# Kernel optimization log

Measured on AMD Instinct MI355X. Metric: run time of the kernel, lower is better.

## Reference

```python
import jax, jax.numpy as jnp
import numpy as np

T, B, D, H = 2048, 4, 1024, 16
DK = D // H
SCALE = 1.0 / np.sqrt(DK)


def setup_inputs() -> dict:
    key = jax.random.key(0)
    k1, k2, k3 = jax.random.split(key, 3)
    x = jax.random.normal(k1, (T, B, D), dtype=jnp.float32)
    # xavier_uniform-ish scaling
    W_qkv = jax.random.normal(k2, (3 * D, D), dtype=jnp.float32) * np.sqrt(2.0 / (D + 3 * D))
    W_out = jax.random.normal(k3, (D, D), dtype=jnp.float32) * np.sqrt(1.0 / D)
    b_out = jnp.zeros((D,), dtype=jnp.float32)
    return {"x": x, "W_qkv": W_qkv, "W_out": W_out, "b_out": b_out}


def reference(x, W_qkv, W_out, b_out):
    Tn, Bn, Dn = x.shape
    # QKV projection (Linear with weight [3D, D], no bias)
    qkv = x @ W_qkv.T                                  # (T, B, 3D)
    qkv = qkv.reshape(Tn, Bn, 3, H, DK)
    q, k, v = qkv[:, :, 0], qkv[:, :, 1], qkv[:, :, 2]  # each (T, B, H, dk)
    scores = jnp.einsum('tbhd,sbhd->bhts', q, k) * SCALE  # (B, H, T, T)
    causal = jnp.triu(jnp.ones((Tn, Tn), dtype=bool), k=1)
    scores = jnp.where(causal, -jnp.inf, scores)
    attn = jax.nn.softmax(scores, axis=-1)
    out = jnp.einsum('bhts,sbhd->tbhd', attn, v)        # (T, B, H, dk)
    out = out.reshape(Tn, Bn, Dn)
    return out @ W_out.T + b_out
```

## Files before the change

### kernel.cpp

```cpp
#include <hip/hip_runtime.h>
#include <stdint.h>

#define T_DIM 2048
#define B_DIM 4
#define D_DIM 1024
#define H_NUM 16
#define HD 64
#define MROWS (T_DIM * B_DIM)
#define QKV_N (3 * D_DIM)
#define ATT_C 0.18033688011112042f

typedef unsigned short u16;
typedef __bf16 bf16x8 __attribute__((ext_vector_type(8)));
typedef float f32x4 __attribute__((ext_vector_type(4)));
typedef float f32x16 __attribute__((ext_vector_type(16)));
typedef u16 u16x4 __attribute__((ext_vector_type(4)));
typedef u16 u16x8 __attribute__((ext_vector_type(8)));

__device__ __forceinline__ u16 f2bf(float f) {
  union { float f; unsigned u; } v; v.f = f;
  unsigned r = v.u + 0x7fffu + ((v.u >> 16) & 1u);
  return (u16)(r >> 16);
}

__device__ __forceinline__ void async_copy16(void* lds, const void* g) {
  __builtin_amdgcn_global_load_lds((__attribute__((address_space(1))) void*)(g),
                                   (__attribute__((address_space(3))) void*)(lds),
                                   16, 0, 0);
}

__global__ __launch_bounds__(256) void cast3_f32_bf16(
    const float* __restrict__ s0, const float* __restrict__ s1,
    const float* __restrict__ s2, u16* __restrict__ dst,
    int n0, int n01, int ntot4) {
  int i = blockIdx.x * 256 + threadIdx.x;
  if (i >= ntot4) return;
  int e = i * 4;
  const float* s; int off;
  if (e < n0) { s = s0; off = 0; }
  else if (e < n01) { s = s1; off = n0; }
  else { s = s2; off = n01; }
  float4 v = *reinterpret_cast<const float4*>(s + (e - off));
  u16x4 o = {f2bf(v.x), f2bf(v.y), f2bf(v.z), f2bf(v.w)};
  *reinterpret_cast<u16x4*>(dst + e) = o;
}

template <int OUT_F32_BIAS>
__global__ __launch_bounds__(256) void gemm_bt(
    const u16* __restrict__ A, const u16* __restrict__ Bm,
    u16* __restrict__ Cb, float* __restrict__ Cf, const float* __restrict__ bias,
    int M, int N, int K) {
  __shared__ __attribute__((aligned(16))) u16 As[128 * 64];
  __shared__ __attribute__((aligned(16))) u16 Bs[128 * 64];

  const int tid = threadIdx.x;
  const int lane = tid & 63, wid = tid >> 6;
  const int l15 = lane & 15, lg = lane >> 4;
  const int wr = wid >> 1, wc = wid & 1;
  const int m0 = blockIdx.y * 128, n0 = blockIdx.x * 128;

  f32x4 acc[4][4];
#pragma unroll
  for (int i = 0; i < 4; i++)
#pragma unroll
    for (int j = 0; j < 4; j++) acc[i][j] = (f32x4){0.f, 0.f, 0.f, 0.f};

  const int srow = tid >> 3;
  const int scol = (tid & 7) * 8;
  const u16* gA = A + (size_t)(m0 + srow) * K + scol;
  const u16* gB = Bm + (size_t)(n0 + srow) * K + scol;
  u16* lA = As + tid * 8;
  u16* lB = Bs + tid * 8;

  const int KT = K >> 6;
  for (int kt = 0; kt < KT; ++kt) {
    const int kofs = kt * 64;
#pragma unroll
    for (int p = 0; p < 4; ++p) {
      async_copy16(lA + p * 256 * 8, gA + (size_t)(p * 32) * K + kofs);
      async_copy16(lB + p * 256 * 8, gB + (size_t)(p * 32) * K + kofs);
    }
    __syncthreads();
#pragma unroll
    for (int kk = 0; kk < 2; ++kk) {
      bf16x8 af[4], bfr[4];
#pragma unroll
      for (int mt = 0; mt < 4; ++mt)
        af[mt] = *reinterpret_cast<const bf16x8*>(
            &As[(wr * 64 + mt * 16 + l15) * 64 + kk * 32 + lg * 8]);
#pragma unroll
      for (int nt = 0; nt < 4; ++nt)
        bfr[nt] = *reinterpret_cast<const bf16x8*>(
            &Bs[(wc * 64 + nt * 16 + l15) * 64 + kk * 32 + lg * 8]);
#pragma unroll
      for (int mt = 0; mt < 4; ++mt)
#pragma unroll
        for (int nt = 0; nt < 4; ++nt)
          acc[mt][nt] = __builtin_amdgcn_mfma_f32_16x16x32_bf16(
              af[mt], bfr[nt], acc[mt][nt], 0, 0, 0);
    }
    __syncthreads();
  }

  const float qsc = (!OUT_F32_BIAS && n0 < D_DIM) ? ATT_C : 1.0f;
#pragma unroll
  for (int mt = 0; mt < 4; ++mt) {
#pragma unroll
    for (int r = 0; r < 4; ++r) {
      const int row = m0 + wr * 64 + mt * 16 + lg * 4 + r;
#pragma unroll
      for (int nt = 0; nt < 4; ++nt) {
        const int col = n0 + wc * 64 + nt * 16 + l15;
        float v = acc[mt][nt][r];
        if (OUT_F32_BIAS) {
          Cf[(size_t)row * N + col] = v + bias[col];
        } else {
          Cb[(size_t)row * N + col] = f2bf(v * qsc);
        }
      }
    }
  }
}

#define VF_STRIDE 24
#define VF_FRAG (32 * VF_STRIDE)

__device__ __forceinline__ void process32(
    const bf16x8 (&qf)[4], f32x16 (&o)[2], f32x16& lacc,
    int q0w, int kv0, int l31, int hi, bool needMask, const bf16x8 onesf,
    const u16* __restrict__ Ks, const u16* __restrict__ Vf) {
  f32x16 s[2];
#pragma unroll
  for (int kb = 0; kb < 2; ++kb)
#pragma unroll
    for (int r = 0; r < 16; ++r) s[kb][r] = 0.f;

  __builtin_amdgcn_s_setprio(1);
#pragma unroll
  for (int kb = 0; kb < 2; ++kb) {
#pragma unroll
    for (int ks = 0; ks < 4; ++ks) {
      const int row = kb * 32 + l31;
      bf16x8 kf = *reinterpret_cast<const bf16x8*>(
          &Ks[row * 64 + ((((ks << 1) | hi)) ^ (l31 & 7)) * 8]);
      s[kb] = __builtin_amdgcn_mfma_f32_32x32x16_bf16(kf, qf[ks], s[kb], 0, 0, 0);
    }
  }
  __builtin_amdgcn_s_setprio(0);

  if (needMask) {
    const int q = q0w + l31;
#pragma unroll
    for (int kb = 0; kb < 2; ++kb)
#pragma unroll
      for (int r = 0; r < 16; ++r) {
        const int kv = kv0 + kb * 32 + (r & 3) + ((r >> 2) << 3) + (hi << 2);
        if (kv > q) s[kb][r] = -1e30f;
      }
  }
#pragma unroll
  for (int kb = 0; kb < 2; ++kb)
#pragma unroll
    for (int r = 0; r < 16; ++r)
      s[kb][r] = __builtin_amdgcn_exp2f(s[kb][r]);

  union Frag { unsigned u[4]; bf16x8 v; };
  Frag pf[4];
#pragma unroll
  for (int kb = 0; kb < 2; ++kb)
#pragma unroll
    for (int g = 0; g < 2; ++g) {
#pragma unroll
      for (int t2 = 0; t2 < 2; ++t2) {
        unsigned x, y;
        asm("v_cvt_pk_bf16_f32 %0, %1, %2"
            : "=v"(x) : "v"(s[kb][g * 8 + t2 * 2]), "v"(s[kb][g * 8 + t2 * 2 + 1]));
        asm("v_cvt_pk_bf16_f32 %0, %1, %2"
            : "=v"(y) : "v"(s[kb][g * 8 + t2 * 2 + 4]), "v"(s[kb][g * 8 + t2 * 2 + 5]));
        asm("v_permlane32_swap_b32 %0, %1" : "+v"(x), "+v"(y));
        pf[kb * 2 + g].u[t2] = x;
        pf[kb * 2 + g].u[t2 + 2] = y;
      }
    }

  __builtin_amdgcn_s_setprio(1);
#pragma unroll
  for (int ks = 0; ks < 4; ++ks) {
    lacc = __builtin_amdgcn_mfma_f32_32x32x16_bf16(onesf, pf[ks].v, lacc, 0, 0, 0);
#pragma unroll
    for (int db = 0; db < 2; ++db) {
      bf16x8 vf = *reinterpret_cast<const bf16x8*>(
          &Vf[(ks * 2 + db) * VF_FRAG + l31 * VF_STRIDE + hi * 8]);
      o[db] = __builtin_amdgcn_mfma_f32_32x32x16_bf16(vf, pf[ks].v, o[db], 0, 0, 0);
    }
  }
  __builtin_amdgcn_s_setprio(0);
}

__global__ __launch_bounds__(256, 2) void attn_kernel(
    const u16* __restrict__ qkv, u16* __restrict__ aout) {
  __shared__ __attribute__((aligned(16))) u16 Ks[128 * 64];
  __shared__ __attribute__((aligned(16))) u16 Vf[16 * VF_FRAG];

  const int tid = threadIdx.x;
  const int lane = tid & 63, w = tid >> 6;
  const int l31 = lane & 31, hi = lane >> 5;

  const int nwg = gridDim.x * gridDim.y;
  const int lin = blockIdx.y * gridDim.x + blockIdx.x;
  const int swz = (lin & 7) * (nwg >> 3) + (lin >> 3);
  const int px = swz % gridDim.x;
  const int bh = swz / gridDim.x;
  const int b = bh >> 4, h = bh & 15;
  const int qtA = px, qtB = 15 - px;
  const int q0A = qtA * 128 + w * 32, q0B = qtB * 128 + w * 32;

  bf16x8 qfA[4], qfB[4];
  {
    const u16* pA = qkv + ((size_t)(q0A + l31) * B_DIM + b) * QKV_N + h * HD + hi * 8;
    const u16* pB = qkv + ((size_t)(q0B + l31) * B_DIM + b) * QKV_N + h * HD + hi * 8;
#pragma unroll
    for (int ks = 0; ks < 4; ++ks) {
      qfA[ks] = *reinterpret_cast<const bf16x8*>(pA + ks * 16);
      qfB[ks] = *reinterpret_cast<const bf16x8*>(pB + ks * 16);
    }
  }

  bf16x8 onesf;
  {
    union { u16 u[8]; bf16x8 v; } ou;
#pragma unroll
    for (int i = 0; i < 8; ++i) ou.u[i] = 0x3F80;
    onesf = ou.v;
  }

  f32x16 oA[2], oB[2], laccA, laccB;
#pragma unroll
  for (int r = 0; r < 16; ++r) { laccA[r] = 0.f; laccB[r] = 0.f; }
#pragma unroll
  for (int db = 0; db < 2; ++db)
#pragma unroll
    for (int r = 0; r < 16; ++r) { oA[db][r] = 0.f; oB[db][r] = 0.f; }

  const int srow = tid >> 3;
  const int scol = (tid & 7) * 8;
  const int csw = (tid & 7) ^ (srow & 7);

  for (int kt2 = 0; kt2 <= qtB; ++kt2) {
    const int base = kt2 * 128;
#pragma unroll
    for (int p = 0; p < 4; ++p) {
      const u16* gK = qkv + ((size_t)(base + p * 32 + srow) * B_DIM + b) * QKV_N +
                      D_DIM + h * HD + csw * 8;
      async_copy16(Ks + tid * 8 + p * 2048, gK);
    }
    u16x8 vv[4];
#pragma unroll
    for (int p = 0; p < 4; ++p) {
      const u16* gV = qkv + ((size_t)(base + p * 32 + srow) * B_DIM + b) * QKV_N +
                      2 * D_DIM + h * HD + scol;
      vv[p] = *reinterpret_cast<const u16x8*>(gV);
    }
#pragma unroll
    for (int p = 0; p < 4; ++p) {
      const int kvl = p * 32 + srow;
      const int fb = (kvl >> 4) * 2;
      const int e16 = kvl & 15;
#pragma unroll
      for (int jj = 0; jj < 8; ++jj) {
        const int j = (jj + srow) & 7;
        const int d = scol + j;
        Vf[(fb + (d >> 5)) * VF_FRAG + (d & 31) * VF_STRIDE + e16] = vv[p][j];
      }
    }
    __syncthreads();

#pragma unroll
    for (int half = 0; half < 2; ++half) {
      const int kv0 = base + half * 64;
      const u16* Kh = Ks + half * (64 * 64);
      const u16* Vh = Vf + half * 8 * VF_FRAG;
      if (kv0 <= q0A + 31)
        process32(qfA, oA, laccA, q0A, kv0, l31, hi, kv0 + 63 > q0A, onesf, Kh, Vh);
      if (kv0 <= q0B + 31)
        process32(qfB, oB, laccB, q0B, kv0, l31, hi, kv0 + 63 > q0B, onesf, Kh, Vh);
    }
    __syncthreads();
  }

#pragma unroll
  for (int t = 0; t < 2; ++t) {
    const float inv = 1.0f / (t == 0 ? laccA[0] : laccB[0]);
    const int q0w = t == 0 ? q0A : q0B;
    f32x16* o = t == 0 ? oA : oB;
    u16* orow = aout + ((size_t)(q0w + l31) * B_DIM + b) * D_DIM + h * HD;
#pragma unroll
    for (int db = 0; db < 2; ++db)
#pragma unroll
      for (int rq = 0; rq < 4; ++rq) {
        u16x4 o4;
#pragma unroll
        for (int e = 0; e < 4; ++e) o4[e] = f2bf(o[db][rq * 4 + e] * inv);
        *reinterpret_cast<u16x4*>(orow + db * 32 + rq * 8 + hi * 4) = o4;
      }
  }
}

extern "C" void kernel_launch(void* const* d_in, const int* in_sizes, int n_in,
                              void* d_out, int out_size, void* d_ws, size_t ws_size,
                              hipStream_t stream) {
  (void)in_sizes; (void)n_in; (void)out_size; (void)ws_size;
  const float* x = (const float*)d_in[0];
  const float* Wqkv = (const float*)d_in[1];
  const float* Wout = (const float*)d_in[2];
  const float* bout = (const float*)d_in[3];
  float* out = (float*)d_out;

  u16* xb = (u16*)d_ws;
  u16* wqkvb = xb + (size_t)MROWS * D_DIM;
  u16* woutb = wqkvb + (size_t)QKV_N * D_DIM;
  u16* qkv = woutb + (size_t)D_DIM * D_DIM;
  u16* aout = qkv + (size_t)MROWS * QKV_N;

  {
    const int n0 = MROWS * D_DIM;
    const int n01 = n0 + QKV_N * D_DIM;
    const int ntot = n01 + D_DIM * D_DIM;
    const int n4 = ntot / 4;
    cast3_f32_bf16<<<(n4 + 255) / 256, 256, 0, stream>>>(
        x, Wqkv, Wout, xb, n0, n01, n4);
  }

  gemm_bt<0><<<dim3(QKV_N / 128, MROWS / 128), 256, 0, stream>>>(
      xb, wqkvb, qkv, nullptr, nullptr, MROWS, QKV_N, D_DIM);

  attn_kernel<<<dim3(8, B_DIM * H_NUM), 256, 0, stream>>>(qkv, aout);

  gemm_bt<1><<<dim3(D_DIM / 128, MROWS / 128), 256, 0, stream>>>(
      aout, woutb, nullptr, out, bout, MROWS, D_DIM, D_DIM);
}
```

Baseline: 192.9 us.

## Replace QKV GEMM with 256x256 tiled, 8-wave pipelined async-copy kernel

Adds a dedicated QKV projection kernel that uses 256x256 output tiles, 512 threads, 128KB dynamic LDS double-buffered with async global-to-LDS copies, XOR-swizzled LDS layout and an interleaved schedule of LDS loads, prefetches and MFMA quarters separated by barriers. A grid swizzle groups workgroups for better L2 reuse. The Q scaling moves from the generic GEMM into this kernel. The aim is higher MFMA utilization and less load latency exposure in the largest GEMM, at the cost of one workgroup per CU and more barriers.

```diff
diff --git a/kernel.cpp b/kernel.cpp
--- a/kernel.cpp
+++ b/kernel.cpp
@@ -102,7 +102,6 @@
     __syncthreads();
   }
 
-  const float qsc = (!OUT_F32_BIAS && n0 < D_DIM) ? ATT_C : 1.0f;
 #pragma unroll
   for (int mt = 0; mt < 4; ++mt) {
 #pragma unroll
@@ -115,11 +114,171 @@
         if (OUT_F32_BIAS) {
           Cf[(size_t)row * N + col] = v + bias[col];
         } else {
-          Cb[(size_t)row * N + col] = f2bf(v * qsc);
+          Cb[(size_t)row * N + col] = f2bf(v);
         }
       }
     }
   }
+}
+
+__global__ __launch_bounds__(512, 1) void gemm_bt8_qkv(
+    const u16* __restrict__ A, const u16* __restrict__ Bm,
+    u16* __restrict__ Cb, int M, int N, int K) {
+  extern __shared__ u16 sm[];
+
+  const int tid = threadIdx.x;
+  const int lane = tid & 63, wid = tid >> 6;
+  const int wr = wid >> 2, wc = wid & 3;
+  const int l15 = lane & 15, lg = lane >> 4;
+  const int xr = ((l15 >> 2) & 1) << 4;
+
+  const int nwg = gridDim.x * gridDim.y;
+  const int lin = blockIdx.y * gridDim.x + blockIdx.x;
+  const int swz = (lin & 7) * (nwg >> 3) + (lin >> 3);
+  const int bx = swz % gridDim.x, by = swz / gridDim.x;
+  const int m0 = by * 256, n0 = bx * 256;
+
+  const int srow = tid >> 3;
+  const int kxs = ((tid & 7) * 8) ^ (((tid >> 5) & 1) << 4);
+  const u16* gA = A + (size_t)(m0 + srow) * K + kxs;
+  const u16* gB = Bm + (size_t)(n0 + srow) * K + kxs;
+
+#define STG(op_, h_, tk_, c_)                                                   \
+  {                                                                             \
+    const u16* g_ = ((op_) ? gB : gA) + (size_t)((h_) * 128) * K + (size_t)(tk_) * 64; \
+    u16* d_ = sm + (c_) * 32768 + (op_) * 16384 + (h_) * 8192 + tid * 8;        \
+    async_copy16(d_, g_);                                                       \
+    async_copy16(d_ + 4096, g_ + (size_t)64 * K);                               \
+  }
+
+#define LDA_(mt_, kk_, c_)                                                      \
+  (*reinterpret_cast<const bf16x8*>(sm + (c_) * 32768 + wr * 8192 +             \
+      ((mt_) * 16 + l15) * 64 + (((kk_) * 32 + lg * 8) ^ xr)))
+#define LDB_(nt_, kk_, c_)                                                      \
+  (*reinterpret_cast<const bf16x8*>(sm + (c_) * 32768 + 16384 + (wc >> 1) * 8192 + \
+      ((wc & 1) * 64 + (nt_) * 16 + l15) * 64 + (((kk_) * 32 + lg * 8) ^ xr)))
+
+  f32x4 acc[8][4];
+#pragma unroll
+  for (int i = 0; i < 8; i++)
+#pragma unroll
+    for (int j = 0; j < 4; j++) acc[i][j] = (f32x4){0.f, 0.f, 0.f, 0.f};
+
+  const int NT = K >> 6;
+
+  STG(0, 0, 0, 0) STG(0, 1, 0, 0) STG(1, 0, 0, 0) STG(1, 1, 0, 0)
+  STG(0, 0, 1, 1) STG(0, 1, 1, 1)
+  asm volatile("s_waitcnt vmcnt(4)" ::: "memory");
+  __builtin_amdgcn_sched_barrier(0);
+  __builtin_amdgcn_s_barrier();
+
+  for (int t = 0; t < NT; ++t) {
+    const int c = t & 1;
+    bf16x8 a03[4][2], a47[4][2], b01[2][2], b23[2][2];
+#pragma unroll
+    for (int mt = 0; mt < 4; ++mt) {
+      a03[mt][0] = LDA_(mt, 0, c);
+      a03[mt][1] = LDA_(mt, 1, c);
+    }
+#pragma unroll
+    for (int nt = 0; nt < 2; ++nt) {
+      b01[nt][0] = LDB_(nt, 0, c);
+      b01[nt][1] = LDB_(nt, 1, c);
+    }
+    if (t + 1 < NT) STG(1, 0, t + 1, c ^ 1)
+    __builtin_amdgcn_s_barrier();
+    asm volatile("s_waitcnt lgkmcnt(0)" ::: "memory");
+    __builtin_amdgcn_sched_barrier(0);
+    __builtin_amdgcn_s_setprio(1);
+#pragma unroll
+    for (int mt = 0; mt < 4; ++mt)
+#pragma unroll
+      for (int nt = 0; nt < 2; ++nt)
+#pragma unroll
+        for (int kk = 0; kk < 2; ++kk)
+          acc[mt][nt] = __builtin_amdgcn_mfma_f32_16x16x32_bf16(
+              a03[mt][kk], b01[nt][kk], acc[mt][nt], 0, 0, 0);
+    __builtin_amdgcn_s_setprio(0);
+    __builtin_amdgcn_s_barrier();
+#pragma unroll
+    for (int mt = 0; mt < 4; ++mt) {
+      a47[mt][0] = LDA_(mt + 4, 0, c);
+      a47[mt][1] = LDA_(mt + 4, 1, c);
+    }
+    if (t + 1 < NT) STG(1, 1, t + 1, c ^ 1)
+    __builtin_amdgcn_s_barrier();
+    asm volatile("s_waitcnt lgkmcnt(0)" ::: "memory");
+    __builtin_amdgcn_sched_barrier(0);
+    __builtin_amdgcn_s_setprio(1);
+#pragma unroll
+    for (int mt = 0; mt < 4; ++mt)
+#pragma unroll
+      for (int nt = 0; nt < 2; ++nt)
+#pragma unroll
+        for (int kk = 0; kk < 2; ++kk)
+          acc[mt + 4][nt] = __builtin_amdgcn_mfma_f32_16x16x32_bf16(
+              a47[mt][kk], b01[nt][kk], acc[mt + 4][nt], 0, 0, 0);
+    __builtin_amdgcn_s_setprio(0);
+    __builtin_amdgcn_s_barrier();
+#pragma unroll
+    for (int nt = 0; nt < 2; ++nt) {
+      b23[nt][0] = LDB_(nt + 2, 0, c);
+      b23[nt][1] = LDB_(nt + 2, 1, c);
+    }
+    if (t + 2 < NT) STG(0, 0, t + 2, c)
+    __builtin_amdgcn_s_barrier();
+    asm volatile("s_waitcnt lgkmcnt(0)" ::: "memory");
+    __builtin_amdgcn_sched_barrier(0);
+    __builtin_amdgcn_s_setprio(1);
+#pragma unroll
+    for (int mt = 0; mt < 4; ++mt)
+#pragma unroll
+      for (int nt = 0; nt < 2; ++nt)
+#pragma unroll
+        for (int kk = 0; kk < 2; ++kk)
+          acc[mt][nt + 2] = __builtin_amdgcn_mfma_f32_16x16x32_bf16(
+              a03[mt][kk], b23[nt][kk], acc[mt][nt + 2], 0, 0, 0);
+    __builtin_amdgcn_s_setprio(0);
+    __builtin_amdgcn_s_barrier();
+    if (t + 2 < NT) STG(0, 1, t + 2, c)
+    __builtin_amdgcn_s_barrier();
+    __builtin_amdgcn_s_setprio(1);
+#pragma unroll
+    for (int mt = 0; mt < 4; ++mt)
+#pragma unroll
+      for (int nt = 0; nt < 2; ++nt)
+#pragma unroll
+        for (int kk = 0; kk < 2; ++kk)
+          acc[mt + 4][nt + 2] = __builtin_amdgcn_mfma_f32_16x16x32_bf16(
+              a47[mt][kk], b23[nt][kk], acc[mt + 4][nt + 2], 0, 0, 0);
+    __builtin_amdgcn_s_setprio(0);
+    if (t + 1 < NT) {
+      if (t + 2 < NT) {
+        asm volatile("s_waitcnt vmcnt(4)" ::: "memory");
+      } else {
+        asm volatile("s_waitcnt vmcnt(0)" ::: "memory");
+      }
+      __builtin_amdgcn_sched_barrier(0);
+    }
+    __builtin_amdgcn_s_barrier();
+  }
+
+  const float qsc = (n0 < D_DIM) ? ATT_C : 1.0f;
+#pragma unroll
+  for (int mt = 0; mt < 8; ++mt) {
+#pragma unroll
+    for (int r = 0; r < 4; ++r) {
+      const int row = m0 + wr * 128 + mt * 16 + lg * 4 + r;
+#pragma unroll
+      for (int nt = 0; nt < 4; ++nt) {
+        const int col = n0 + wc * 64 + nt * 16 + l15;
+        Cb[(size_t)row * N + col] = f2bf(acc[mt][nt][r] * qsc);
+      }
+    }
+  }
+#undef STG
+#undef LDA_
+#undef LDB_
 }
 
 #define VF_STRIDE 24
@@ -331,8 +490,10 @@
         x, Wqkv, Wout, xb, n0, n01, n4);
   }
 
-  gemm_bt<0><<<dim3(QKV_N / 128, MROWS / 128), 256, 0, stream>>>(
-      xb, wqkvb, qkv, nullptr, nullptr, MROWS, QKV_N, D_DIM);
+  hipFuncSetAttribute((const void*)gemm_bt8_qkv,
+                      hipFuncAttributeMaxDynamicSharedMemorySize, 131072);
+  gemm_bt8_qkv<<<dim3(QKV_N / 256, MROWS / 256), 512, 131072, stream>>>(
+      xb, wqkvb, qkv, MROWS, QKV_N, D_DIM);
 
   attn_kernel<<<dim3(8, B_DIM * H_NUM), 256, 0, stream>>>(qkv, aout);
 
```

Result: no change. 189.7 us (-1.7%).
